# Optimization experiments

Measured on AMD Instinct MI355X. Metric: run time of the kernel, lower is better.

The kernel has to match this reference:

```python
import jax, jax.numpy as jnp
import numpy as np

E = 800_000      # number of edges
DIN = 128        # in_channels
DMID = 256       # mid_channels
DOUT = 128       # output_channels
V = 50_000       # number of vertices (segments)


def setup_inputs() -> dict:
    key = jax.random.key(0)
    k1, k2, k3, k4, k5 = jax.random.split(key, 5)
    x = jax.random.normal(k1, (E, DIN), dtype=jnp.float32)
    vertex_id = jax.random.randint(k2, (E,), 0, V)
    W1 = jax.random.normal(k3, (DIN, DMID), dtype=jnp.float32) * (1.0 / np.sqrt(DIN))
    b1 = jax.random.normal(k4, (DMID,), dtype=jnp.float32) * 0.01
    W2 = jax.random.normal(k5, (DIN + DMID, DOUT), dtype=jnp.float32) * (1.0 / np.sqrt(DIN + DMID))
    return {"x": x, "vertex_id": vertex_id, "W1": W1, "b1": b1, "W2": W2, "num_vertices": V}


def reference(x, vertex_id, W1, b1, W2, num_vertices):
    # first_process: Linear(DIN -> DMID)                        (E, DMID)
    z = x @ W1 + b1
    # aggregator: scatter_max over vertex segments              (V, DMID)
    z_max = jax.ops.segment_max(z, vertex_id, num_segments=num_vertices)
    # formatter: index_select gather back to edges              (E, DMID)
    z_vertex = jnp.take(z_max, vertex_id, axis=0)
    # merger: concat along feature dim                          (E, DIN+DMID)
    z_merged = jnp.concatenate([x, z_vertex], axis=-1)
    # second_process: Linear(DIN+DMID -> DOUT, bias=False)      (E, DOUT)
    return z_merged @ W2
```

## Files before the change

### kernel.cpp

```cpp
#include <hip/hip_runtime.h>

#define DIN   128
#define DMID  256
#define DOUT  128
#define VNUM  50000

typedef __attribute__((ext_vector_type(8))) __bf16 bf16x8;
typedef __attribute__((ext_vector_type(4))) float  f32x4;

static __device__ __forceinline__ unsigned short b16(float f) {
  union { __bf16 b; unsigned short u; } r; r.b = (__bf16)f; return r.u;
}
static __device__ __forceinline__ unsigned pk2(float lo, float hi) {
  union { __bf16 b[2]; unsigned u; } r;
  r.b[0] = (__bf16)lo; r.b[1] = (__bf16)hi;
  return r.u;
}
static __device__ __forceinline__ unsigned unflip_bits(unsigned m) {
  unsigned mask = ((int)m < 0) ? 0x80000000u : 0xFFFFFFFFu;
  return m ^ mask;
}
static __device__ __forceinline__ unsigned flip32_from16(unsigned m) {
  return (m << 16) | ((m & 0x8000u) ? 0u : 0xFFFFu);
}

#define LBAR() do {                                            \
    __builtin_amdgcn_sched_barrier(0);                         \
    asm volatile("s_waitcnt lgkmcnt(0)" ::: "memory");         \
    __builtin_amdgcn_sched_barrier(0);                         \
    __builtin_amdgcn_s_barrier();                              \
    __builtin_amdgcn_sched_barrier(0);                         \
  } while (0)

__global__ __launch_bounds__(256) void k_zero(uint4* __restrict__ p, int n16) {
  const int stride = gridDim.x * 256;
  const uint4 z = {0u, 0u, 0u, 0u};
  for (int i = blockIdx.x * 256 + threadIdx.x; i < n16; i += stride) p[i] = z;
}

__global__ void k_hist(const int* __restrict__ vid, int* __restrict__ counts, int E) {
  int i = blockIdx.x * blockDim.x + threadIdx.x;
  if (i < E) atomicAdd(counts + vid[i], 1);
}

__global__ __launch_bounds__(256) void k_scan_red(
    const int* __restrict__ cnt, int* __restrict__ bsum, int V) {
  __shared__ int ws[4];
  const int i = blockIdx.x * 256 + threadIdx.x;
  int c = (i < V) ? cnt[i] : 0;
#pragma unroll
  for (int d = 1; d < 64; d <<= 1) c += __shfl_xor(c, d);
  if ((threadIdx.x & 63) == 0) ws[threadIdx.x >> 6] = c;
  __syncthreads();
  if (threadIdx.x == 0) bsum[blockIdx.x] = ws[0] + ws[1] + ws[2] + ws[3];
}

__global__ __launch_bounds__(256) void k_scan_top(int* __restrict__ bsum, int nb) {
  __shared__ int ws[4];
  const int tid = threadIdx.x, lane = tid & 63, wv = tid >> 6;
  int c = (tid < nb) ? bsum[tid] : 0;
  int s = c;
#pragma unroll
  for (int d = 1; d < 64; d <<= 1) {
    int u = __shfl_up(s, d, 64);
    if (lane >= d) s += u;
  }
  if (lane == 63) ws[wv] = s;
  __syncthreads();
  int off = 0;
  for (int k = 0; k < wv; ++k) off += ws[k];
  if (tid < nb) bsum[tid] = off + (s - c);
}

__global__ __launch_bounds__(256) void k_scan_fix(
    int* __restrict__ cursor, const int* __restrict__ bsum, int V) {
  __shared__ int ws[4];
  const int i = blockIdx.x * 256 + threadIdx.x;
  const int lane = threadIdx.x & 63, wv = threadIdx.x >> 6;
  int c = (i < V) ? cursor[i] : 0;
  int s = c;
#pragma unroll
  for (int d = 1; d < 64; d <<= 1) {
    int u = __shfl_up(s, d, 64);
    if (lane >= d) s += u;
  }
  if (lane == 63) ws[wv] = s;
  __syncthreads();
  int off = bsum[blockIdx.x];
  for (int k = 0; k < wv; ++k) off += ws[k];
  if (i < V) cursor[i] = off + (s - c);
}

__global__ void k_scatter(const int* __restrict__ vid, int* __restrict__ cursor,
                          int* __restrict__ sorted, int E) {
  int i = blockIdx.x * blockDim.x + threadIdx.x;
  if (i < E) {
    int v = vid[i];
    int p = atomicAdd(cursor + v, 1);
    sorted[p] = i;
  }
}

#define K1_ITER(TT, CA0, CA1, CA2, CA3, CAV, CAM, IB0, IB1, IB2, IB3, IBV, IBM, PCUR) \
  {                                                                                    \
                                   \
    IBM = (TT + 2 * G) < ntiles;                                                       \
    if (IBM) {                                                                         \
      const float4* _src =                                                             \
          reinterpret_cast<const float4*>(x + (size_t)eidI * DIN + s8 * 16);           \
      IB0 = _src[0]; IB1 = _src[1]; IB2 = _src[2]; IB3 = _src[3];                      \
      if (tid < 32) IBV = vid[sidI];                                                   \
    }                                                                                  \
    if ((TT + 3 * G) < ntiles) {                        \
      eidI = sorted[(TT + 3 * G) * 32 + row8];                                         \
      if (tid < 32) sidI = sorted[(TT + 3 * G) * 32 + tid];                            \
    }                                                                                  \
                                                \
    const int _myv = lvid[PCUR][r32];                                                  \
    const int _nv  = (r32 == 31) ? (_myv ^ 1) : lvid[PCUR][r32 + 1];                   \
    const unsigned _emask = (unsigned)(__ballot(_myv != _nv) & 0xFFFFFFFFull);         \
                                                  \
    f32x4 _acc[2][4];                                                                  \
    _Pragma("unroll") for (int mi = 0; mi < 2; ++mi)                                   \
      _Pragma("unroll") for (int ni = 0; ni < 4; ++ni)                                 \
        _acc[mi][ni] = (f32x4){bias[ni], bias[ni], bias[ni], bias[ni]};                \
    _Pragma("unroll") for (int kk = 0; kk < 4; ++kk) {                                 \
      bf16x8 _a[2];                                                                    \
      _Pragma("unroll") for (int mi = 0; mi < 2; ++mi)                                 \
        _a[mi] = *reinterpret_cast<const bf16x8*>(                                     \
            &lx[(mi * 16 + l15) * 136 + kk * 32 + l4 * 8]);                            \
      _Pragma("unroll") for (int mi = 0; mi < 2; ++mi)                                 \
        _Pragma("unroll") for (int ni = 0; ni < 4; ++ni)                               \
          _acc[mi][ni] = __builtin_amdgcn_mfma_f32_16x16x32_bf16(                      \
              _a[mi], bfrag[kk][ni], _acc[mi][ni], 0, 0, 0);                           \
    }                                                                                  \
                     \
    _Pragma("unroll") for (int ni = 0; ni < 4; ++ni) {                                 \
      const int _col = w * 64 + ni * 16 + l15;                                         \
      const int _cb  = _col * 17 + l4 * 2;                                             \
      _Pragma("unroll") for (int mi = 0; mi < 2; ++mi)                                 \
        _Pragma("unroll") for (int p = 0; p < 2; ++p) {                                \
          unsigned _tpk = pk2(_acc[mi][ni][2 * p], _acc[mi][ni][2 * p + 1]);           \
          unsigned _mf = 0x80008000u + ((_tpk >> 15) & 0x00010001u) * 0x7FFFu;         \
          zt[_cb + mi * 8 + p] = _tpk ^ _mf;                                           \
        }                                                                              \
    }                                                                                  \
    LBAR();                                                                            \
               \
    if (CAM) {                                                                         \
      uint2 _o0 = { pk2(CA0.x, CA0.y), pk2(CA0.z, CA0.w) };                            \
      uint2 _o1 = { pk2(CA1.x, CA1.y), pk2(CA1.z, CA1.w) };                            \
      uint2 _o2 = { pk2(CA2.x, CA2.y), pk2(CA2.z, CA2.w) };                            \
      uint2 _o3 = { pk2(CA3.x, CA3.y), pk2(CA3.z, CA3.w) };                            \
      unsigned short* _dst = &lx[row8 * 136 + s8 * 16];                                \
      *reinterpret_cast<uint2*>(_dst + 0)  = _o0;                                      \
      *reinterpret_cast<uint2*>(_dst + 4)  = _o1;                                      \
      *reinterpret_cast<uint2*>(_dst + 8)  = _o2;                                      \
      *reinterpret_cast<uint2*>(_dst + 12) = _o3;                                      \
      if (tid < 32) lvid[PCUR ^ 1][tid] = CAV;                                         \
    }                                                                                  \
    __builtin_amdgcn_sched_barrier(0);                                                 \
                      \
    {                                                                                  \
      const int _colw = tid;                                                           \
      const unsigned* _zc = &zt[_colw * 17];                                           \
      unsigned _curm = 0;                                                              \
      bool _first = true;                                                              \
      _Pragma("unroll") for (int p = 0; p < 16; ++p) {                                 \
        const unsigned _pr = _zc[p];                                                   \
        _Pragma("unroll") for (int j = 0; j < 2; ++j) {                                \
          const unsigned _val = j ? (_pr >> 16) : (_pr & 0xFFFFu);                     \
          _curm = _val > _curm ? _val : _curm;                                         \
          const int _row = p * 2 + j;                                                  \
          if ((_emask >> _row) & 1) {                                                  \
            const int _v = lvid[PCUR][_row];                                           \
            const unsigned _enc = flip32_from16(_curm);                                \
            unsigned* _ad = zu + (size_t)_v * DMID + _colw;                            \
            if (_first || _row == 31) atomicMax(_ad, _enc);                            \
            else *_ad = _enc;                                                          \
            _curm = 0; _first = false;                                                 \
          }                                                                            \
        }                                                                              \
      }                                                                                \
    }                                                                                  \
    LBAR();                                                                            \
  }

__global__ __launch_bounds__(256) void k_gemm1_max(
    const float* __restrict__ x, const int* __restrict__ vid,
    const int* __restrict__ sorted, const float* __restrict__ W1,
    const float* __restrict__ b1, unsigned* __restrict__ zu, int ntiles) {
  __shared__ unsigned short lx[32 * 136];
  __shared__ unsigned zt[256 * 17];
  __shared__ int lvid[2][32];

  const int tid  = threadIdx.x;
  const int lane = tid & 63;
  const int w    = tid >> 6;
  const int l15  = lane & 15;
  const int l4   = lane >> 4;
  const int r32  = lane & 31;
  const int row8 = tid >> 3;
  const int s8   = tid & 7;
  const int G    = gridDim.x;

  bf16x8 bfrag[4][4];
  float  bias[4];
#pragma unroll
  for (int ni = 0; ni < 4; ++ni) {
    const int col = w * 64 + ni * 16 + l15;
    bias[ni] = b1[col];
#pragma unroll
    for (int kk = 0; kk < 4; ++kk) {
      union { bf16x8 v; unsigned short u[8]; } tmp;
#pragma unroll
      for (int j = 0; j < 8; ++j)
        tmp.u[j] = b16(W1[(kk * 32 + l4 * 8 + j) * DMID + col]);
      bfrag[kk][ni] = tmp.v;
    }
  }

  const int t0 = blockIdx.x;
  if (t0 >= ntiles) return;

  {
    if (tid < 32) lvid[0][tid] = vid[sorted[t0 * 32 + tid]];
    const int eid = sorted[t0 * 32 + row8];
    const float4* src =
        reinterpret_cast<const float4*>(x + (size_t)eid * DIN + s8 * 16);
#pragma unroll
    for (int i = 0; i < 4; ++i) {
      float4 v = src[i];
      uint2 o = { pk2(v.x, v.y), pk2(v.z, v.w) };
      *reinterpret_cast<uint2*>(&lx[row8 * 136 + s8 * 16 + i * 4]) = o;
    }
  }
  float4 a0, a1, a2, a3, b0, b1c, b2, b3;
  int vA = 0, vB = 0;
  bool mA = (t0 + G) < ntiles, mB = false;
  if (mA) {
    const int eidA = sorted[(t0 + G) * 32 + row8];
    const float4* src =
        reinterpret_cast<const float4*>(x + (size_t)eidA * DIN + s8 * 16);
    a0 = src[0]; a1 = src[1]; a2 = src[2]; a3 = src[3];
    if (tid < 32) vA = vid[sorted[(t0 + G) * 32 + tid]];
  }
  int eidI = 0, sidI = 0;
  if ((t0 + 2 * G) < ntiles) {
    eidI = sorted[(t0 + 2 * G) * 32 + row8];
    if (tid < 32) sidI = sorted[(t0 + 2 * G) * 32 + tid];
  }
  __syncthreads();

  int t = t0;
  while (t < ntiles) {
    K1_ITER(t, a0, a1, a2, a3, vA, mA, b0, b1c, b2, b3, vB, mB, 0);
    t += G;
    if (t >= ntiles) break;
    K1_ITER(t, b0, b1c, b2, b3, vB, mB, a0, a1, a2, a3, vA, mA, 1);
    t += G;
  }
}

__global__ __launch_bounds__(256) void k_ymm(
    const unsigned* __restrict__ zu, const float* __restrict__ W2,
    float* __restrict__ Y, int ntiles) {
  extern __shared__ unsigned short sm[];
  unsigned short* w2bt = sm;
  unsigned short* za   = sm + 128 * 264;

  const int tid  = threadIdx.x;
  const int lane = tid & 63;
  const int w    = tid >> 6;
  const int wr   = w >> 1, wc = w & 1;
  const int l15  = lane & 15, l4 = lane >> 4;

  {
    const int n = tid & 127, kh = tid >> 7;
    for (int k = kh * 128; k < kh * 128 + 128; ++k)
      w2bt[n * 264 + k] = b16(W2[(size_t)(DIN + k) * DOUT + n]);
  }
  __syncthreads();

  for (int t = blockIdx.x; t < ntiles; t += gridDim.x) {
    {
      const int row = tid >> 2, q = tid & 3;
      const int v = t * 64 + row;
      unsigned short* dz = &za[row * 264 + q * 64];
      if (v < VNUM) {
        const uint4* sz = reinterpret_cast<const uint4*>(zu + (size_t)v * DMID + q * 64);
#pragma unroll
        for (int i = 0; i < 16; ++i) {
          uint4 m = sz[i];
          ushort4 o = { (unsigned short)(unflip_bits(m.x) >> 16),
                        (unsigned short)(unflip_bits(m.y) >> 16),
                        (unsigned short)(unflip_bits(m.z) >> 16),
                        (unsigned short)(unflip_bits(m.w) >> 16) };
          *reinterpret_cast<ushort4*>(dz + i * 4) = o;
        }
      } else {
        ushort4 zo = {0, 0, 0, 0};
#pragma unroll
        for (int i = 0; i < 16; ++i) *reinterpret_cast<ushort4*>(dz + i * 4) = zo;
      }
    }
    __syncthreads();

    f32x4 acc[2][4];
#pragma unroll
    for (int mi = 0; mi < 2; ++mi)
#pragma unroll
      for (int ni = 0; ni < 4; ++ni) acc[mi][ni] = (f32x4){0.f, 0.f, 0.f, 0.f};

#pragma unroll
    for (int kk = 0; kk < 8; ++kk) {
      bf16x8 a[2], b[4];
#pragma unroll
      for (int mi = 0; mi < 2; ++mi)
        a[mi] = *reinterpret_cast<const bf16x8*>(
            &za[(wr * 32 + mi * 16 + l15) * 264 + kk * 32 + l4 * 8]);
#pragma unroll
      for (int ni = 0; ni < 4; ++ni)
        b[ni] = *reinterpret_cast<const bf16x8*>(
            &w2bt[(wc * 64 + ni * 16 + l15) * 264 + kk * 32 + l4 * 8]);
#pragma unroll
      for (int mi = 0; mi < 2; ++mi)
#pragma unroll
        for (int ni = 0; ni < 4; ++ni)
          acc[mi][ni] = __builtin_amdgcn_mfma_f32_16x16x32_bf16(
              a[mi], b[ni], acc[mi][ni], 0, 0, 0);
    }

#pragma unroll
    for (int mi = 0; mi < 2; ++mi)
#pragma unroll
      for (int r = 0; r < 4; ++r) {
        const int v = t * 64 + wr * 32 + mi * 16 + l4 * 4 + r;
        if (v < VNUM) {
          float* o = Y + (size_t)v * DOUT + wc * 64 + l15;
#pragma unroll
          for (int ni = 0; ni < 4; ++ni) o[ni * 16] = acc[mi][ni][r];
        }
      }
    __syncthreads();
  }
}

__global__ __launch_bounds__(256) void k_gemm2(
    const float* __restrict__ x, const int* __restrict__ vid,
    const float* __restrict__ W2, const float* __restrict__ Y,
    float* __restrict__ out, int ntiles) {
  __shared__ unsigned short w2at[128 * 136];
  __shared__ unsigned short lx[64 * 136];
  __shared__ int lvid[64];

  const int tid  = threadIdx.x;
  const int lane = tid & 63;
  const int w    = tid >> 6;
  const int wr   = w >> 1, wc = w & 1;
  const int l15  = lane & 15, l4 = lane >> 4;

  {
    const int n = tid & 127, kh = tid >> 7;
    for (int k = kh * 64; k < kh * 64 + 64; ++k)
      w2at[n * 136 + k] = b16(W2[(size_t)k * DOUT + n]);
  }
  __syncthreads();

  for (int t = blockIdx.x; t < ntiles; t += gridDim.x) {
    {
      const int row = tid >> 2, q = tid & 3;
      const float4* sx =
          reinterpret_cast<const float4*>(x + (size_t)(t * 64 + row) * DIN + q * 32);
#pragma unroll
      for (int i = 0; i < 8; ++i) {
        float4 v = sx[i];
        uint2 o = { pk2(v.x, v.y), pk2(v.z, v.w) };
        *reinterpret_cast<uint2*>(&lx[row * 136 + q * 32 + i * 4]) = o;
      }
      if (tid < 64) lvid[tid] = vid[t * 64 + tid];
    }
    LBAR();

    float yv[2][4][4];
#pragma unroll
    for (int mi = 0; mi < 2; ++mi)
#pragma unroll
      for (int r = 0; r < 4; ++r) {
        const int row = wr * 32 + mi * 16 + l4 * 4 + r;
        const float* Yr = Y + (size_t)lvid[row] * DOUT + wc * 64 + l15;
#pragma unroll
        for (int ni = 0; ni < 4; ++ni) yv[mi][r][ni] = Yr[ni * 16];
      }

    f32x4 acc[2][4];
#pragma unroll
    for (int mi = 0; mi < 2; ++mi)
#pragma unroll
      for (int ni = 0; ni < 4; ++ni) acc[mi][ni] = (f32x4){0.f, 0.f, 0.f, 0.f};

#pragma unroll
    for (int kk = 0; kk < 4; ++kk) {
      bf16x8 a[2], b[4];
#pragma unroll
      for (int mi = 0; mi < 2; ++mi)
        a[mi] = *reinterpret_cast<const bf16x8*>(
            &lx[(wr * 32 + mi * 16 + l15) * 136 + kk * 32 + l4 * 8]);
#pragma unroll
      for (int ni = 0; ni < 4; ++ni)
        b[ni] = *reinterpret_cast<const bf16x8*>(
            &w2at[(wc * 64 + ni * 16 + l15) * 136 + kk * 32 + l4 * 8]);
#pragma unroll
      for (int mi = 0; mi < 2; ++mi)
#pragma unroll
        for (int ni = 0; ni < 4; ++ni)
          acc[mi][ni] = __builtin_amdgcn_mfma_f32_16x16x32_bf16(
              a[mi], b[ni], acc[mi][ni], 0, 0, 0);
    }

#pragma unroll
    for (int mi = 0; mi < 2; ++mi)
#pragma unroll
      for (int r = 0; r < 4; ++r) {
        const int row = wr * 32 + mi * 16 + l4 * 4 + r;
        float* o = out + (size_t)(t * 64 + row) * DOUT + wc * 64 + l15;
#pragma unroll
        for (int ni = 0; ni < 4; ++ni) o[ni * 16] = acc[mi][ni][r] + yv[mi][r][ni];
      }
    LBAR();
  }
}

extern "C" void kernel_launch(void* const* d_in, const int* in_sizes, int n_in,
                              void* d_out, int out_size, void* d_ws, size_t ws_size,
                              hipStream_t stream) {
  const float* x   = (const float*)d_in[0];
  const int*   vid = (const int*)d_in[1];
  const float* W1  = (const float*)d_in[2];
  const float* b1  = (const float*)d_in[3];
  const float* W2  = (const float*)d_in[4];
  float* out = (float*)d_out;

  const int E = in_sizes[1];
  const int ntiles32 = E / 32;
  const int ntiles64 = E / 64;
  const int ntY = (VNUM + 63) / 64;
  const int nb = (VNUM + 255) / 256;

  char* ws = (char*)d_ws;
  size_t off = 0;
  unsigned* zu = (unsigned*)(ws + off); off += (size_t)VNUM * DMID * 4;
  int* cnt     = (int*)(ws + off);      off += (size_t)VNUM * 4;
  int* sorted  = (int*)(ws + off);      off += (size_t)E * 4;
  float* Y     = (float*)(ws + off);    off += (size_t)VNUM * DOUT * 4;
  int* bsum    = (int*)(ws + off);      off += 4096;

  const int n16 = (int)(((size_t)VNUM * DMID * 4 + VNUM * 4) / 16);
  k_zero<<<2048, 256, 0, stream>>>((uint4*)zu, n16);

  k_hist<<<(E + 255) / 256, 256, 0, stream>>>(vid, cnt, E);
  k_scan_red<<<nb, 256, 0, stream>>>(cnt, bsum, VNUM);
  k_scan_top<<<1, 256, 0, stream>>>(bsum, nb);
  k_scan_fix<<<nb, 256, 0, stream>>>(cnt, bsum, VNUM);
  k_scatter<<<(E + 255) / 256, 256, 0, stream>>>(vid, cnt, sorted, E);

  k_gemm1_max<<<1024, 256, 0, stream>>>(x, vid, sorted, W1, b1, zu, ntiles32);

  const int smY = (128 * 264 + 64 * 264) * sizeof(unsigned short);
  hipFuncSetAttribute((const void*)k_ymm,
                      hipFuncAttributeMaxDynamicSharedMemorySize, smY);
  k_ymm<<<782, 256, smY, stream>>>(zu, W2, Y, ntY);

  k_gemm2<<<768, 256, 0, stream>>>(x, vid, W2, Y, out, ntiles64);
}
```

Before: 545.0 us.

## Fuse zero, histogram, scan and scatter into one cooperative kernel

Replaces six small launches (zeroing, histogram, three-phase scan, scatter) with a single cooperative kernel that uses grid-wide syncs between phases. The intent is to remove per-launch overhead and inter-kernel gaps in the counting-sort preprocessing. In exchange, each phase now runs on only 512 blocks with grid-stride loops, and every grid.sync adds a barrier cost.

New measurement: 823.3 us. 51.1% more time.

```diff
diff --git a/kernel.cpp b/kernel.cpp
--- a/kernel.cpp
+++ b/kernel.cpp
@@ -1,9 +1,13 @@
 #include <hip/hip_runtime.h>
+#include <hip/hip_cooperative_groups.h>
+
+namespace cg = cooperative_groups;
 
 #define DIN   128
 #define DMID  256
 #define DOUT  128
 #define VNUM  50000
+#define NCH   196
 
 typedef __attribute__((ext_vector_type(8))) __bf16 bf16x8;
 typedef __attribute__((ext_vector_type(4))) float  f32x4;
@@ -32,71 +36,68 @@
     __builtin_amdgcn_sched_barrier(0);                         \
   } while (0)
 
-__global__ __launch_bounds__(256) void k_zero(uint4* __restrict__ p, int n16) {
-  const int stride = gridDim.x * 256;
-  const uint4 z = {0u, 0u, 0u, 0u};
-  for (int i = blockIdx.x * 256 + threadIdx.x; i < n16; i += stride) p[i] = z;
-}
-
-__global__ void k_hist(const int* __restrict__ vid, int* __restrict__ counts, int E) {
-  int i = blockIdx.x * blockDim.x + threadIdx.x;
-  if (i < E) atomicAdd(counts + vid[i], 1);
-}
-
-__global__ __launch_bounds__(256) void k_scan_red(
-    const int* __restrict__ cnt, int* __restrict__ bsum, int V) {
-  __shared__ int ws[4];
-  const int i = blockIdx.x * 256 + threadIdx.x;
-  int c = (i < V) ? cnt[i] : 0;
-#pragma unroll
-  for (int d = 1; d < 64; d <<= 1) c += __shfl_xor(c, d);
-  if ((threadIdx.x & 63) == 0) ws[threadIdx.x >> 6] = c;
-  __syncthreads();
-  if (threadIdx.x == 0) bsum[blockIdx.x] = ws[0] + ws[1] + ws[2] + ws[3];
-}
-
-__global__ __launch_bounds__(256) void k_scan_top(int* __restrict__ bsum, int nb) {
-  __shared__ int ws[4];
-  const int tid = threadIdx.x, lane = tid & 63, wv = tid >> 6;
-  int c = (tid < nb) ? bsum[tid] : 0;
-  int s = c;
-#pragma unroll
-  for (int d = 1; d < 64; d <<= 1) {
-    int u = __shfl_up(s, d, 64);
-    if (lane >= d) s += u;
-  }
-  if (lane == 63) ws[wv] = s;
-  __syncthreads();
-  int off = 0;
-  for (int k = 0; k < wv; ++k) off += ws[k];
-  if (tid < nb) bsum[tid] = off + (s - c);
-}
-
-__global__ __launch_bounds__(256) void k_scan_fix(
-    int* __restrict__ cursor, const int* __restrict__ bsum, int V) {
-  __shared__ int ws[4];
-  const int i = blockIdx.x * 256 + threadIdx.x;
-  const int lane = threadIdx.x & 63, wv = threadIdx.x >> 6;
-  int c = (i < V) ? cursor[i] : 0;
-  int s = c;
-#pragma unroll
-  for (int d = 1; d < 64; d <<= 1) {
-    int u = __shfl_up(s, d, 64);
-    if (lane >= d) s += u;
-  }
-  if (lane == 63) ws[wv] = s;
-  __syncthreads();
-  int off = bsum[blockIdx.x];
-  for (int k = 0; k < wv; ++k) off += ws[k];
-  if (i < V) cursor[i] = off + (s - c);
-}
-
-__global__ void k_scatter(const int* __restrict__ vid, int* __restrict__ cursor,
-                          int* __restrict__ sorted, int E) {
-  int i = blockIdx.x * blockDim.x + threadIdx.x;
-  if (i < E) {
-    int v = vid[i];
-    int p = atomicAdd(cursor + v, 1);
+__global__ __launch_bounds__(256) void k_sort(
+    const int* __restrict__ vid, int* __restrict__ cnt, int* __restrict__ bsum,
+    int* __restrict__ sorted, unsigned* __restrict__ zu, int E) {
+  cg::grid_group grid = cg::this_grid();
+  __shared__ int ws4[4];
+  const int tid = threadIdx.x;
+  const int gid = blockIdx.x * 256 + tid;
+  const int gsz = gridDim.x * 256;
+  const int lane = tid & 63, wv = tid >> 6;
+
+  {
+    const int n16 = (int)(((size_t)VNUM * DMID * 4 + VNUM * 4) / 16);
+    uint4* p = reinterpret_cast<uint4*>(zu);
+    const uint4 z = {0u, 0u, 0u, 0u};
+    for (int i = gid; i < n16; i += gsz) p[i] = z;
+  }
+  grid.sync();
+
+  for (int i = gid; i < E; i += gsz) atomicAdd(cnt + vid[i], 1);
+  grid.sync();
+
+  for (int c = blockIdx.x; c < NCH; c += gridDim.x) {
+    const int i = c * 256 + tid;
+    const int v = (i < VNUM) ? cnt[i] : 0;
+    int s = v;
+#pragma unroll
+    for (int d = 1; d < 64; d <<= 1) {
+      int u = __shfl_up(s, d, 64);
+      if (lane >= d) s += u;
+    }
+    if (lane == 63) ws4[wv] = s;
+    __syncthreads();
+    int off = 0;
+    for (int k = 0; k < wv; ++k) off += ws4[k];
+    if (i < VNUM) cnt[i] = off + s - v;
+    if (tid == 255) bsum[c] = off + s;
+    __syncthreads();
+  }
+  grid.sync();
+
+  if (blockIdx.x == 0) {
+    const int v = (tid < NCH) ? bsum[tid] : 0;
+    int s = v;
+#pragma unroll
+    for (int d = 1; d < 64; d <<= 1) {
+      int u = __shfl_up(s, d, 64);
+      if (lane >= d) s += u;
+    }
+    if (lane == 63) ws4[wv] = s;
+    __syncthreads();
+    int off = 0;
+    for (int k = 0; k < wv; ++k) off += ws4[k];
+    if (tid < NCH) bsum[tid] = off + s - v;
+  }
+  grid.sync();
+
+  for (int i = gid; i < VNUM; i += gsz) cnt[i] += bsum[i >> 8];
+  grid.sync();
+
+  for (int i = gid; i < E; i += gsz) {
+    const int v = vid[i];
+    const int p = atomicAdd(cnt + v, 1);
     sorted[p] = i;
   }
 }
@@ -445,7 +446,6 @@
   const int ntiles32 = E / 32;
   const int ntiles64 = E / 64;
   const int ntY = (VNUM + 63) / 64;
-  const int nb = (VNUM + 255) / 256;
 
   char* ws = (char*)d_ws;
   size_t off = 0;
@@ -455,14 +455,12 @@
   float* Y     = (float*)(ws + off);    off += (size_t)VNUM * DOUT * 4;
   int* bsum    = (int*)(ws + off);      off += 4096;
 
-  const int n16 = (int)(((size_t)VNUM * DMID * 4 + VNUM * 4) / 16);
-  k_zero<<<2048, 256, 0, stream>>>((uint4*)zu, n16);
-
-  k_hist<<<(E + 255) / 256, 256, 0, stream>>>(vid, cnt, E);
-  k_scan_red<<<nb, 256, 0, stream>>>(cnt, bsum, VNUM);
-  k_scan_top<<<1, 256, 0, stream>>>(bsum, nb);
-  k_scan_fix<<<nb, 256, 0, stream>>>(cnt, bsum, VNUM);
-  k_scatter<<<(E + 255) / 256, 256, 0, stream>>>(vid, cnt, sorted, E);
+  {
+    void* args[] = { (void*)&vid, (void*)&cnt, (void*)&bsum,
+                     (void*)&sorted, (void*)&zu, (void*)&E };
+    hipLaunchCooperativeKernel((void*)k_sort, dim3(512), dim3(256),
+                               args, 0, stream);
+  }
 
   k_gemm1_max<<<1024, 256, 0, stream>>>(x, vid, sorted, W1, b1, zu, ntiles32);
 
```
